# Kernel optimization log

Hardware: AMD Instinct MI355X
Metric: run time of the kernel (lower is better)

The kernel has to match this reference:

```python
import jax, jax.numpy as jnp
import numpy as np

N_NODES = 100000


def gcn_conv(x, edge_index, W, b, n_nodes):
    """PyG GCNConv: add self-loops, symmetric deg^-1/2 normalization,
    linear transform, scatter-add aggregate, bias."""
    src, dst = edge_index[0], edge_index[1]
    # add self-loops
    loop = jnp.arange(n_nodes, dtype=edge_index.dtype)
    src = jnp.concatenate([src, loop])
    dst = jnp.concatenate([dst, loop])
    # transform first (in_dim >= out_dim ordering used by PyG)
    h = x @ W  # [N, out]
    # symmetric normalization from in-degree (incl. self-loops)
    ones = jnp.ones(src.shape[0], dtype=x.dtype)
    deg = jax.ops.segment_sum(ones, dst, num_segments=n_nodes)
    dinv = jnp.where(deg > 0, jax.lax.rsqrt(deg), 0.0).astype(x.dtype)
    norm = dinv[src] * dinv[dst]  # [E+N]
    msg = h[src] * norm[:, None]  # gather + scale
    out = jax.ops.segment_sum(msg, dst, num_segments=n_nodes)
    return out + b


def setup_inputs() -> dict:
    key = jax.random.key(0)
    k1, k2, k3, k4 = jax.random.split(key, 4)
    n, e = N_NODES, 1600000
    d_in, d_hid, n_cls = 256, 256, 64
    x = jax.random.normal(k1, (n, d_in), dtype=jnp.float32)
    edge_index = jax.random.randint(k2, (2, e), 0, n, dtype=jnp.int64)
    W1 = jax.random.normal(k3, (d_in, d_hid), dtype=jnp.float32) / np.sqrt(d_in)
    b1 = jnp.zeros((d_hid,), dtype=jnp.float32)
    W2 = jax.random.normal(k4, (d_hid, n_cls), dtype=jnp.float32) / np.sqrt(d_hid)
    b2 = jnp.zeros((n_cls,), dtype=jnp.float32)
    return {"x": x, "edge_index": edge_index, "W1": W1, "b1": b1, "W2": W2, "b2": b2}


def reference(x, edge_index, W1, b1, W2, b2):
    n = x.shape[0]
    h = jax.nn.relu(gcn_conv(x, edge_index, W1, b1, n))
    # dropout is identity in eval mode (training=False)
    logits = gcn_conv(h, edge_index, W2, b2, n)
    return jax.nn.log_softmax(logits, axis=1)
```

## Files before the change

kernel.cpp:

```cpp
#include <hip/hip_runtime.h>
#include <math.h>


typedef __attribute__((ext_vector_type(8))) short bf16x8;
typedef __attribute__((ext_vector_type(4))) float f32x4;

__device__ inline unsigned short f2bf(float f) {
    union { float f; unsigned int u; } v; v.f = f;
    unsigned int r = v.u + 0x7fffu + ((v.u >> 16) & 1u);
    return (unsigned short)(r >> 16);
}
__device__ inline float bfu2f(unsigned short u) {
    union { unsigned int u; float f; } v; v.u = ((unsigned int)u) << 16; return v.f;
}
__device__ inline float bf2f_lo(unsigned int u) {
    union { unsigned int u; float f; } v; v.u = u << 16; return v.f;
}
__device__ inline float bf2f_hi(unsigned int u) {
    union { unsigned int u; float f; } v; v.u = u & 0xffff0000u; return v.f;
}

__global__ __launch_bounds__(256) void deg_count_kernel(
    const int* __restrict__ dst, int E, int* __restrict__ cnt) {
    int e = blockIdx.x * blockDim.x + threadIdx.x;
    if (e < E) atomicAdd(&cnt[dst[e]], 1);
}

__global__ __launch_bounds__(256) void scan_part1_kernel(
    const int* __restrict__ cnt, int* __restrict__ bsum, int N) {
    __shared__ int s[256];
    const int tid = threadIdx.x;
    int base = blockIdx.x * 1024 + tid * 4;
    int v = 0;
#pragma unroll
    for (int j = 0; j < 4; ++j)
        if (base + j < N) v += cnt[base + j];
    s[tid] = v;
    __syncthreads();
    for (int off = 128; off > 0; off >>= 1) {
        if (tid < off) s[tid] += s[tid + off];
        __syncthreads();
    }
    if (tid == 0) bsum[blockIdx.x] = s[0];
}

__global__ __launch_bounds__(1024) void scan_part2_kernel(
    const int* __restrict__ bsum, int* __restrict__ boffs, int NB,
    int* __restrict__ row_ptr, int N) {
    __shared__ int s[1024];
    const int tid = threadIdx.x;
    int v = (tid < NB) ? bsum[tid] : 0;
    s[tid] = v;
    __syncthreads();
    for (int off = 1; off < 1024; off <<= 1) {
        int t = (tid >= off) ? s[tid - off] : 0;
        __syncthreads();
        if (tid >= off) s[tid] += t;
        __syncthreads();
    }
    if (tid < NB) boffs[tid] = s[tid] - v;
    if (tid == 1023) row_ptr[N] = s[1023];
}

__global__ __launch_bounds__(256) void scan_part3_kernel(
    const int* __restrict__ cnt, const int* __restrict__ boffs,
    int* __restrict__ row_ptr, int* __restrict__ cursor, int N) {
    __shared__ int s[256];
    const int tid = threadIdx.x;
    int base = blockIdx.x * 1024 + tid * 4;
    int c[4];
    int v = 0;
#pragma unroll
    for (int j = 0; j < 4; ++j) {
        c[j] = (base + j < N) ? cnt[base + j] : 0;
        v += c[j];
    }
    s[tid] = v;
    __syncthreads();
    for (int off = 1; off < 256; off <<= 1) {
        int t = (tid >= off) ? s[tid - off] : 0;
        __syncthreads();
        if (tid >= off) s[tid] += t;
        __syncthreads();
    }
    int run = boffs[blockIdx.x] + s[tid] - v;
#pragma unroll
    for (int j = 0; j < 4; ++j) {
        if (base + j < N) {
            row_ptr[base + j] = run;
            cursor[base + j] = run;
            run += c[j];
        }
    }
}

__global__ __launch_bounds__(256) void scatter_kernel(
    const int* __restrict__ src, const int* __restrict__ dst,
    const int* __restrict__ cnt, int* __restrict__ cursor,
    int2* __restrict__ csr_ew, int E) {
    int e = blockIdx.x * blockDim.x + threadIdx.x;
    if (e >= E) return;
    int s = src[e], d = dst[e];
    float w = rsqrtf((float)cnt[s] + 1.0f) * rsqrtf((float)cnt[d] + 1.0f);
    int pos = atomicAdd(&cursor[d], 1);
    int2 rec;
    rec.x = s;
    rec.y = __float_as_int(w);
    csr_ew[pos] = rec;
}

__global__ __launch_bounds__(256) void castw_kernel(
    const float* __restrict__ W, unsigned short* __restrict__ Wt,
    int K, int Ncol) {
    int i = blockIdx.x * 256 + threadIdx.x;
    if (i < K * Ncol) {
        int n = i / K;
        int k = i - n * K;
        Wt[i] = f2bf(W[(size_t)k * Ncol + n]);
    }
}

__global__ __launch_bounds__(256) void gemm1_kernel(
    const float* __restrict__ A, const unsigned short* __restrict__ Bt,
    unsigned short* __restrict__ C, int M) {
    __shared__ unsigned short As[64][32];
    __shared__ unsigned short Bs[256][32];

    const int tid = threadIdx.x;
    const int wave = tid >> 6, lane = tid & 63;
    const int quad = lane >> 4, l15 = lane & 15;
    const int m0 = blockIdx.x * 64;

    f32x4 acc[4][4] = {};

    const int arow = tid >> 2;
    const int akk = (tid & 3) << 3;
    const int gr = m0 + arow;

    for (int k0 = 0; k0 < 256; k0 += 32) {
        float4 a0 = make_float4(0.f, 0.f, 0.f, 0.f), a1 = a0;
        if (gr < M) {
            a0 = *(const float4*)&A[(size_t)gr * 256 + k0 + akk];
            a1 = *(const float4*)&A[(size_t)gr * 256 + k0 + akk + 4];
        }
        bf16x8 av;
        av[0] = (short)f2bf(a0.x); av[1] = (short)f2bf(a0.y);
        av[2] = (short)f2bf(a0.z); av[3] = (short)f2bf(a0.w);
        av[4] = (short)f2bf(a1.x); av[5] = (short)f2bf(a1.y);
        av[6] = (short)f2bf(a1.z); av[7] = (short)f2bf(a1.w);
        *(bf16x8*)&As[arow][akk] = av;

        const unsigned short* bsrc = &Bt[(size_t)tid * 256 + k0];
        *(bf16x8*)&Bs[tid][0]  = *(const bf16x8*)&bsrc[0];
        *(bf16x8*)&Bs[tid][8]  = *(const bf16x8*)&bsrc[8];
        *(bf16x8*)&Bs[tid][16] = *(const bf16x8*)&bsrc[16];
        *(bf16x8*)&Bs[tid][24] = *(const bf16x8*)&bsrc[24];
        __syncthreads();

        bf16x8 af[4], bfv[4];
#pragma unroll
        for (int mt = 0; mt < 4; ++mt)
            af[mt] = *(const bf16x8*)&As[mt * 16 + l15][quad * 8];
#pragma unroll
        for (int nt = 0; nt < 4; ++nt)
            bfv[nt] = *(const bf16x8*)&Bs[wave * 64 + nt * 16 + l15][quad * 8];
#pragma unroll
        for (int mt = 0; mt < 4; ++mt)
#pragma unroll
            for (int nt = 0; nt < 4; ++nt)
                acc[mt][nt] = __builtin_amdgcn_mfma_f32_16x16x32_bf16(
                    af[mt], bfv[nt], acc[mt][nt], 0, 0, 0);
        __syncthreads();
    }

#pragma unroll
    for (int mt = 0; mt < 4; ++mt) {
#pragma unroll
        for (int nt = 0; nt < 4; ++nt) {
            int gcol = wave * 64 + nt * 16 + l15;
#pragma unroll
            for (int r = 0; r < 4; ++r) {
                int grow = m0 + mt * 16 + quad * 4 + r;
                if (grow < M)
                    C[(size_t)grow * 256 + gcol] = f2bf(acc[mt][nt][r]);
            }
        }
    }
}

__global__ __launch_bounds__(256) void agg256b_kernel(
    const uint2* __restrict__ h, const int2* __restrict__ ew,
    const int* __restrict__ row_ptr, const int* __restrict__ cnt,
    const float* __restrict__ bias, uint2* __restrict__ outb, int N) {
    const int node = blockIdx.x * 4 + (threadIdx.x >> 6);
    if (node >= N) return;
    const int lane = threadIdx.x & 63;

    float dv = rsqrtf((float)cnt[node] + 1.0f);
    float w0 = dv * dv;
    uint2 p = h[(size_t)node * 64 + lane];
    float4 acc;
    acc.x = bf2f_lo(p.x) * w0; acc.y = bf2f_hi(p.x) * w0;
    acc.z = bf2f_lo(p.y) * w0; acc.w = bf2f_hi(p.y) * w0;

    const int beg = row_ptr[node], end = row_ptr[node + 1];
    int e = beg;
    for (; e + 4 <= end; e += 4) {
        int2 p0 = ew[e];
        int2 p1 = ew[e + 1];
        int2 p2 = ew[e + 2];
        int2 p3 = ew[e + 3];
        uint2 q0 = h[(size_t)p0.x * 64 + lane];
        uint2 q1 = h[(size_t)p1.x * 64 + lane];
        uint2 q2 = h[(size_t)p2.x * 64 + lane];
        uint2 q3 = h[(size_t)p3.x * 64 + lane];
        float w0_ = __int_as_float(p0.y), w1_ = __int_as_float(p1.y);
        float w2_ = __int_as_float(p2.y), w3_ = __int_as_float(p3.y);
        acc.x += bf2f_lo(q0.x) * w0_ + bf2f_lo(q1.x) * w1_ +
                 bf2f_lo(q2.x) * w2_ + bf2f_lo(q3.x) * w3_;
        acc.y += bf2f_hi(q0.x) * w0_ + bf2f_hi(q1.x) * w1_ +
                 bf2f_hi(q2.x) * w2_ + bf2f_hi(q3.x) * w3_;
        acc.z += bf2f_lo(q0.y) * w0_ + bf2f_lo(q1.y) * w1_ +
                 bf2f_lo(q2.y) * w2_ + bf2f_lo(q3.y) * w3_;
        acc.w += bf2f_hi(q0.y) * w0_ + bf2f_hi(q1.y) * w1_ +
                 bf2f_hi(q2.y) * w2_ + bf2f_hi(q3.y) * w3_;
    }
    for (; e < end; ++e) {
        int2 pe = ew[e];
        float w = __int_as_float(pe.y);
        uint2 q = h[(size_t)pe.x * 64 + lane];
        acc.x += bf2f_lo(q.x) * w; acc.y += bf2f_hi(q.x) * w;
        acc.z += bf2f_lo(q.y) * w; acc.w += bf2f_hi(q.y) * w;
    }

    float4 b = *(const float4*)&bias[lane * 4];
    unsigned int o0 = f2bf(fmaxf(acc.x + b.x, 0.f));
    unsigned int o1 = f2bf(fmaxf(acc.y + b.y, 0.f));
    unsigned int o2 = f2bf(fmaxf(acc.z + b.z, 0.f));
    unsigned int o3 = f2bf(fmaxf(acc.w + b.w, 0.f));
    uint2 ov;
    ov.x = o0 | (o1 << 16);
    ov.y = o2 | (o3 << 16);
    outb[(size_t)node * 64 + lane] = ov;
}

__global__ __launch_bounds__(256) void gemm2_kernel(
    const unsigned short* __restrict__ Ab, const unsigned short* __restrict__ Bt,
    unsigned short* __restrict__ C, int M) {
    __shared__ unsigned short As[64][32];
    __shared__ unsigned short Bs[64][32];

    const int tid = threadIdx.x;
    const int wave = tid >> 6, lane = tid & 63;
    const int quad = lane >> 4, l15 = lane & 15;
    const int m0 = blockIdx.x * 64;

    f32x4 acc[4] = {};

    const int arow = tid >> 2;
    const int akk = (tid & 3) << 3;
    const int gr = m0 + arow;
    const int bn = tid & 63, bkc = (tid >> 6) << 3;

    for (int k0 = 0; k0 < 256; k0 += 32) {
        bf16x8 av = {};
        if (gr < M) av = *(const bf16x8*)&Ab[(size_t)gr * 256 + k0 + akk];
        *(bf16x8*)&As[arow][akk] = av;
        *(bf16x8*)&Bs[bn][bkc] = *(const bf16x8*)&Bt[(size_t)bn * 256 + k0 + bkc];
        __syncthreads();

        bf16x8 af = *(const bf16x8*)&As[wave * 16 + l15][quad * 8];
#pragma unroll
        for (int nt = 0; nt < 4; ++nt) {
            bf16x8 bfv = *(const bf16x8*)&Bs[nt * 16 + l15][quad * 8];
            acc[nt] = __builtin_amdgcn_mfma_f32_16x16x32_bf16(af, bfv, acc[nt], 0, 0, 0);
        }
        __syncthreads();
    }

#pragma unroll
    for (int nt = 0; nt < 4; ++nt) {
#pragma unroll
        for (int r = 0; r < 4; ++r) {
            int grow = m0 + wave * 16 + quad * 4 + r;
            if (grow < M) C[(size_t)grow * 64 + nt * 16 + l15] = f2bf(acc[nt][r]);
        }
    }
}

__global__ __launch_bounds__(256) void agg64_kernel(
    const unsigned short* __restrict__ h, const int2* __restrict__ ew,
    const int* __restrict__ row_ptr, const int* __restrict__ cnt,
    const float* __restrict__ bias, float* __restrict__ out, int N) {
    const int d = blockIdx.x * 4 + (threadIdx.x >> 6);
    if (d >= N) return;
    const int lane = threadIdx.x & 63;

    float dv = rsqrtf((float)cnt[d] + 1.0f);
    float acc = bfu2f(h[(size_t)d * 64 + lane]) * dv * dv;

    const int beg = row_ptr[d], end = row_ptr[d + 1];
    int e = beg;
    for (; e + 4 <= end; e += 4) {
        int2 p0 = ew[e];
        int2 p1 = ew[e + 1];
        int2 p2 = ew[e + 2];
        int2 p3 = ew[e + 3];
        float v0 = bfu2f(h[(size_t)p0.x * 64 + lane]);
        float v1 = bfu2f(h[(size_t)p1.x * 64 + lane]);
        float v2 = bfu2f(h[(size_t)p2.x * 64 + lane]);
        float v3 = bfu2f(h[(size_t)p3.x * 64 + lane]);
        acc += v0 * __int_as_float(p0.y) + v1 * __int_as_float(p1.y) +
               v2 * __int_as_float(p2.y) + v3 * __int_as_float(p3.y);
    }
    for (; e < end; ++e) {
        int2 pe = ew[e];
        acc += bfu2f(h[(size_t)pe.x * 64 + lane]) * __int_as_float(pe.y);
    }

    float v = acc + bias[lane];
    float m = v;
#pragma unroll
    for (int off = 32; off > 0; off >>= 1) m = fmaxf(m, __shfl_xor(m, off, 64));
    float ex = expf(v - m);
    float ssum = ex;
#pragma unroll
    for (int off = 32; off > 0; off >>= 1) ssum += __shfl_xor(ssum, off, 64);
    out[(size_t)d * 64 + lane] = v - m - logf(ssum);
}

extern "C" void kernel_launch(void* const* d_in, const int* in_sizes, int n_in,
                              void* d_out, int out_size, void* d_ws, size_t ws_size,
                              hipStream_t stream) {
    const float* x  = (const float*)d_in[0];
    const int*   ei = (const int*)d_in[1];
    const float* W1 = (const float*)d_in[2];
    const float* b1 = (const float*)d_in[3];
    const float* W2 = (const float*)d_in[4];
    const float* b2 = (const float*)d_in[5];
    float* out = (float*)d_out;

    const int N = in_sizes[0] / 256;
    const int E = in_sizes[1] / 2;
    const int NP = 102400;
    const int NB = (N + 1023) / 1024;

    char* ws = (char*)d_ws;
    int*   cnt     = (int*)ws;                 ws += (size_t)NP * 4;
    int*   cursor  = (int*)ws;                 ws += (size_t)NP * 4;
    int*   row_ptr = (int*)ws;                 ws += (size_t)(NP + 4) * 4;
    int*   bsum    = (int*)ws;                 ws += (size_t)1024 * 4;
    int*   boffs   = (int*)ws;                 ws += (size_t)1024 * 4;
    int2*  csr_ew  = (int2*)ws;                ws += (size_t)E * 8;
    unsigned short* W1t   = (unsigned short*)ws; ws += (size_t)256 * 256 * 2;
    unsigned short* W2t   = (unsigned short*)ws; ws += (size_t)256 * 64 * 2;
    unsigned short* h1b   = (unsigned short*)ws; ws += (size_t)N * 256 * 2;
    unsigned short* agg1b = (unsigned short*)ws; ws += (size_t)N * 256 * 2;
    unsigned short* h2b   = (unsigned short*)ws; ws += (size_t)N * 64 * 2;

    hipMemsetAsync(cnt, 0, (size_t)N * sizeof(int), stream);

    deg_count_kernel<<<(E + 255) / 256, 256, 0, stream>>>(ei + E, E, cnt);
    scan_part1_kernel<<<NB, 256, 0, stream>>>(cnt, bsum, N);
    scan_part2_kernel<<<1, 1024, 0, stream>>>(bsum, boffs, NB, row_ptr, N);
    scan_part3_kernel<<<NB, 256, 0, stream>>>(cnt, boffs, row_ptr, cursor, N);
    scatter_kernel<<<(E + 255) / 256, 256, 0, stream>>>(
        ei, ei + E, cnt, cursor, csr_ew, E);

    castw_kernel<<<(256 * 256 + 255) / 256, 256, 0, stream>>>(W1, W1t, 256, 256);
    castw_kernel<<<(256 * 64 + 255) / 256, 256, 0, stream>>>(W2, W2t, 256, 64);

    const int mblocks = (N + 63) / 64;

    gemm1_kernel<<<mblocks, 256, 0, stream>>>(x, W1t, h1b, N);

    agg256b_kernel<<<(N + 3) / 4, 256, 0, stream>>>(
        (const uint2*)h1b, csr_ew, row_ptr, cnt, b1, (uint2*)agg1b, N);

    gemm2_kernel<<<mblocks, 256, 0, stream>>>(agg1b, W2t, h2b, N);

    agg64_kernel<<<(N + 3) / 4, 256, 0, stream>>>(
        h2b, csr_ew, row_ptr, cnt, b2, out, N);
}
```

Baseline: 598.5 us.

## Widen gather loads to 16 bytes and split edges across lane groups in aggregation

Both aggregation kernels now load 16-byte bf16 chunks per lane and use fewer lanes per feature row. The rest of the wavefront's lanes go to processing different edges in parallel. Partial sums are then combined with cross-lane shuffles. In agg64 the old 2-byte per-lane gathers become 16-byte vector loads, with 8 edges processed concurrently per wave, and the log-softmax is reworked for 8 values per lane. The aim is fewer, wider memory transactions and more gathers in flight, at the cost of shuffle reductions and some idle lanes on low-degree tails.

```diff
diff --git a/kernel.cpp b/kernel.cpp
--- a/kernel.cpp
+++ b/kernel.cpp
@@ -10,14 +10,18 @@
     unsigned int r = v.u + 0x7fffu + ((v.u >> 16) & 1u);
     return (unsigned short)(r >> 16);
 }
-__device__ inline float bfu2f(unsigned short u) {
-    union { unsigned int u; float f; } v; v.u = ((unsigned int)u) << 16; return v.f;
-}
 __device__ inline float bf2f_lo(unsigned int u) {
     union { unsigned int u; float f; } v; v.u = u << 16; return v.f;
 }
 __device__ inline float bf2f_hi(unsigned int u) {
     union { unsigned int u; float f; } v; v.u = u & 0xffff0000u; return v.f;
+}
+
+__device__ inline void acc8(float* acc, uint4 q, float w) {
+    acc[0] += bf2f_lo(q.x) * w; acc[1] += bf2f_hi(q.x) * w;
+    acc[2] += bf2f_lo(q.y) * w; acc[3] += bf2f_hi(q.y) * w;
+    acc[4] += bf2f_lo(q.z) * w; acc[5] += bf2f_hi(q.z) * w;
+    acc[6] += bf2f_lo(q.w) * w; acc[7] += bf2f_hi(q.w) * w;
 }
 
 __global__ __launch_bounds__(256) void deg_count_kernel(
@@ -189,59 +193,71 @@
 }
 
 __global__ __launch_bounds__(256) void agg256b_kernel(
-    const uint2* __restrict__ h, const int2* __restrict__ ew,
+    const uint4* __restrict__ h,
+    const int2* __restrict__ ew,
     const int* __restrict__ row_ptr, const int* __restrict__ cnt,
-    const float* __restrict__ bias, uint2* __restrict__ outb, int N) {
+    const float* __restrict__ bias, uint4* __restrict__ outb, int N) {
     const int node = blockIdx.x * 4 + (threadIdx.x >> 6);
     if (node >= N) return;
     const int lane = threadIdx.x & 63;
+    const int half = lane >> 5;
+    const int c = lane & 31;
 
     float dv = rsqrtf((float)cnt[node] + 1.0f);
     float w0 = dv * dv;
-    uint2 p = h[(size_t)node * 64 + lane];
-    float4 acc;
-    acc.x = bf2f_lo(p.x) * w0; acc.y = bf2f_hi(p.x) * w0;
-    acc.z = bf2f_lo(p.y) * w0; acc.w = bf2f_hi(p.y) * w0;
+
+    float acc[8] = {0.f, 0.f, 0.f, 0.f, 0.f, 0.f, 0.f, 0.f};
+    {
+        uint4 q = h[(size_t)node * 32 + c];
+        acc8(acc, q, half == 0 ? w0 : 0.f);
+    }
 
     const int beg = row_ptr[node], end = row_ptr[node + 1];
     int e = beg;
-    for (; e + 4 <= end; e += 4) {
-        int2 p0 = ew[e];
-        int2 p1 = ew[e + 1];
-        int2 p2 = ew[e + 2];
-        int2 p3 = ew[e + 3];
-        uint2 q0 = h[(size_t)p0.x * 64 + lane];
-        uint2 q1 = h[(size_t)p1.x * 64 + lane];
-        uint2 q2 = h[(size_t)p2.x * 64 + lane];
-        uint2 q3 = h[(size_t)p3.x * 64 + lane];
-        float w0_ = __int_as_float(p0.y), w1_ = __int_as_float(p1.y);
-        float w2_ = __int_as_float(p2.y), w3_ = __int_as_float(p3.y);
-        acc.x += bf2f_lo(q0.x) * w0_ + bf2f_lo(q1.x) * w1_ +
-                 bf2f_lo(q2.x) * w2_ + bf2f_lo(q3.x) * w3_;
-        acc.y += bf2f_hi(q0.x) * w0_ + bf2f_hi(q1.x) * w1_ +
-                 bf2f_hi(q2.x) * w2_ + bf2f_hi(q3.x) * w3_;
-        acc.z += bf2f_lo(q0.y) * w0_ + bf2f_lo(q1.y) * w1_ +
-                 bf2f_lo(q2.y) * w2_ + bf2f_lo(q3.y) * w3_;
-        acc.w += bf2f_hi(q0.y) * w0_ + bf2f_hi(q1.y) * w1_ +
-                 bf2f_hi(q2.y) * w2_ + bf2f_hi(q3.y) * w3_;
-    }
-    for (; e < end; ++e) {
-        int2 pe = ew[e];
-        float w = __int_as_float(pe.y);
-        uint2 q = h[(size_t)pe.x * 64 + lane];
-        acc.x += bf2f_lo(q.x) * w; acc.y += bf2f_hi(q.x) * w;
-        acc.z += bf2f_lo(q.y) * w; acc.w += bf2f_hi(q.y) * w;
-    }
-
-    float4 b = *(const float4*)&bias[lane * 4];
-    unsigned int o0 = f2bf(fmaxf(acc.x + b.x, 0.f));
-    unsigned int o1 = f2bf(fmaxf(acc.y + b.y, 0.f));
-    unsigned int o2 = f2bf(fmaxf(acc.z + b.z, 0.f));
-    unsigned int o3 = f2bf(fmaxf(acc.w + b.w, 0.f));
-    uint2 ov;
-    ov.x = o0 | (o1 << 16);
-    ov.y = o2 | (o3 << 16);
-    outb[(size_t)node * 64 + lane] = ov;
+    for (; e + 8 <= end; e += 8) {
+        int2 r0 = ew[e + 0 + half];
+        int2 r1 = ew[e + 2 + half];
+        int2 r2 = ew[e + 4 + half];
+        int2 r3 = ew[e + 6 + half];
+        uint4 q0 = h[(size_t)r0.x * 32 + c];
+        uint4 q1 = h[(size_t)r1.x * 32 + c];
+        uint4 q2 = h[(size_t)r2.x * 32 + c];
+        uint4 q3 = h[(size_t)r3.x * 32 + c];
+        acc8(acc, q0, __int_as_float(r0.y));
+        acc8(acc, q1, __int_as_float(r1.y));
+        acc8(acc, q2, __int_as_float(r2.y));
+        acc8(acc, q3, __int_as_float(r3.y));
+    }
+    for (; e < end; e += 2) {
+        int idx = e + half;
+        int idxc = min(idx, end - 1);
+        int2 r = ew[idxc];
+        float w = (idx < end) ? __int_as_float(r.y) : 0.f;
+        uint4 q = h[(size_t)r.x * 32 + c];
+        acc8(acc, q, w);
+    }
+
+#pragma unroll
+    for (int k = 0; k < 8; ++k) acc[k] += __shfl_xor(acc[k], 32, 64);
+
+    if (half == 0) {
+        float4 b0 = *(const float4*)&bias[c * 8];
+        float4 b1 = *(const float4*)&bias[c * 8 + 4];
+        unsigned int o0 = f2bf(fmaxf(acc[0] + b0.x, 0.f));
+        unsigned int o1 = f2bf(fmaxf(acc[1] + b0.y, 0.f));
+        unsigned int o2 = f2bf(fmaxf(acc[2] + b0.z, 0.f));
+        unsigned int o3 = f2bf(fmaxf(acc[3] + b0.w, 0.f));
+        unsigned int o4 = f2bf(fmaxf(acc[4] + b1.x, 0.f));
+        unsigned int o5 = f2bf(fmaxf(acc[5] + b1.y, 0.f));
+        unsigned int o6 = f2bf(fmaxf(acc[6] + b1.z, 0.f));
+        unsigned int o7 = f2bf(fmaxf(acc[7] + b1.w, 0.f));
+        uint4 ov;
+        ov.x = o0 | (o1 << 16);
+        ov.y = o2 | (o3 << 16);
+        ov.z = o4 | (o5 << 16);
+        ov.w = o6 | (o7 << 16);
+        outb[(size_t)node * 32 + c] = ov;
+    }
 }
 
 __global__ __launch_bounds__(256) void gemm2_kernel(
@@ -289,44 +305,80 @@
 }
 
 __global__ __launch_bounds__(256) void agg64_kernel(
-    const unsigned short* __restrict__ h, const int2* __restrict__ ew,
-    const int* __restrict__ row_ptr, const int* __restrict__ cnt,
-    const float* __restrict__ bias, float* __restrict__ out, int N) {
-    const int d = blockIdx.x * 4 + (threadIdx.x >> 6);
-    if (d >= N) return;
+    const uint4* __restrict__ h,
+    const int2* __restrict__ ew, const int* __restrict__ row_ptr,
+    const int* __restrict__ cnt, const float* __restrict__ bias,
+    float* __restrict__ out, int N) {
+    const int node = blockIdx.x * 4 + (threadIdx.x >> 6);
+    if (node >= N) return;
     const int lane = threadIdx.x & 63;
-
-    float dv = rsqrtf((float)cnt[d] + 1.0f);
-    float acc = bfu2f(h[(size_t)d * 64 + lane]) * dv * dv;
-
-    const int beg = row_ptr[d], end = row_ptr[d + 1];
+    const int g = lane >> 3;
+    const int c = lane & 7;
+
+    float dv = rsqrtf((float)cnt[node] + 1.0f);
+    float w0 = dv * dv;
+
+    float acc[8] = {0.f, 0.f, 0.f, 0.f, 0.f, 0.f, 0.f, 0.f};
+    {
+        uint4 q = h[(size_t)node * 8 + c];
+        acc8(acc, q, g == 0 ? w0 : 0.f);
+    }
+
+    const int beg = row_ptr[node], end = row_ptr[node + 1];
     int e = beg;
-    for (; e + 4 <= end; e += 4) {
-        int2 p0 = ew[e];
-        int2 p1 = ew[e + 1];
-        int2 p2 = ew[e + 2];
-        int2 p3 = ew[e + 3];
-        float v0 = bfu2f(h[(size_t)p0.x * 64 + lane]);
-        float v1 = bfu2f(h[(size_t)p1.x * 64 + lane]);
-        float v2 = bfu2f(h[(size_t)p2.x * 64 + lane]);
-        float v3 = bfu2f(h[(size_t)p3.x * 64 + lane]);
-        acc += v0 * __int_as_float(p0.y) + v1 * __int_as_float(p1.y) +
-               v2 * __int_as_float(p2.y) + v3 * __int_as_float(p3.y);
-    }
-    for (; e < end; ++e) {
-        int2 pe = ew[e];
-        acc += bfu2f(h[(size_t)pe.x * 64 + lane]) * __int_as_float(pe.y);
-    }
-
-    float v = acc + bias[lane];
-    float m = v;
-#pragma unroll
-    for (int off = 32; off > 0; off >>= 1) m = fmaxf(m, __shfl_xor(m, off, 64));
-    float ex = expf(v - m);
-    float ssum = ex;
-#pragma unroll
-    for (int off = 32; off > 0; off >>= 1) ssum += __shfl_xor(ssum, off, 64);
-    out[(size_t)d * 64 + lane] = v - m - logf(ssum);
+    for (; e + 16 <= end; e += 16) {
+        int2 r0 = ew[e + g];
+        int2 r1 = ew[e + 8 + g];
+        uint4 q0 = h[(size_t)r0.x * 8 + c];
+        uint4 q1 = h[(size_t)r1.x * 8 + c];
+        acc8(acc, q0, __int_as_float(r0.y));
+        acc8(acc, q1, __int_as_float(r1.y));
+    }
+    for (; e < end; e += 8) {
+        int idx = e + g;
+        int idxc = min(idx, end - 1);
+        int2 r = ew[idxc];
+        float w = (idx < end) ? __int_as_float(r.y) : 0.f;
+        uint4 q = h[(size_t)r.x * 8 + c];
+        acc8(acc, q, w);
+    }
+
+#pragma unroll
+    for (int k = 0; k < 8; ++k) {
+        acc[k] += __shfl_xor(acc[k], 8, 64);
+        acc[k] += __shfl_xor(acc[k], 16, 64);
+        acc[k] += __shfl_xor(acc[k], 32, 64);
+    }
+
+    float4 b0 = *(const float4*)&bias[c * 8];
+    float4 b1 = *(const float4*)&bias[c * 8 + 4];
+    float v[8];
+    v[0] = acc[0] + b0.x; v[1] = acc[1] + b0.y;
+    v[2] = acc[2] + b0.z; v[3] = acc[3] + b0.w;
+    v[4] = acc[4] + b1.x; v[5] = acc[5] + b1.y;
+    v[6] = acc[6] + b1.z; v[7] = acc[7] + b1.w;
+
+    float m = v[0];
+#pragma unroll
+    for (int k = 1; k < 8; ++k) m = fmaxf(m, v[k]);
+    m = fmaxf(m, __shfl_xor(m, 1, 64));
+    m = fmaxf(m, __shfl_xor(m, 2, 64));
+    m = fmaxf(m, __shfl_xor(m, 4, 64));
+    float s = 0.f;
+#pragma unroll
+    for (int k = 0; k < 8; ++k) s += expf(v[k] - m);
+    s += __shfl_xor(s, 1, 64);
+    s += __shfl_xor(s, 2, 64);
+    s += __shfl_xor(s, 4, 64);
+    float ls = m + logf(s);
+
+    if (g == 0) {
+        float4 o0, o1;
+        o0.x = v[0] - ls; o0.y = v[1] - ls; o0.z = v[2] - ls; o0.w = v[3] - ls;
+        o1.x = v[4] - ls; o1.y = v[5] - ls; o1.z = v[6] - ls; o1.w = v[7] - ls;
+        *(float4*)&out[(size_t)node * 64 + c * 8] = o0;
+        *(float4*)&out[(size_t)node * 64 + c * 8 + 4] = o1;
+    }
 }
 
 extern "C" void kernel_launch(void* const* d_in, const int* in_sizes, int n_in,
@@ -375,10 +427,10 @@
     gemm1_kernel<<<mblocks, 256, 0, stream>>>(x, W1t, h1b, N);
 
     agg256b_kernel<<<(N + 3) / 4, 256, 0, stream>>>(
-        (const uint2*)h1b, csr_ew, row_ptr, cnt, b1, (uint2*)agg1b, N);
+        (const uint4*)h1b, csr_ew, row_ptr, cnt, b1, (uint4*)agg1b, N);
 
     gemm2_kernel<<<mblocks, 256, 0, stream>>>(agg1b, W2t, h2b, N);
 
     agg64_kernel<<<(N + 3) / 4, 256, 0, stream>>>(
-        h2b, csr_ew, row_ptr, cnt, b2, out, N);
-}
+        (const uint4*)h2b, csr_ew, row_ptr, cnt, b2, out, N);
+}
```

After: 581.7 us. 2.8% less time.
